# Kernel tuning notes

Hardware: AMD Instinct MI355X
Metric: run time of the kernel (lower is better)

The kernel has to match this reference:

```python
import jax, jax.numpy as jnp
import numpy as np
import math

B, SQ, SK = 8, 1024, 1024
DIM_Q = DIM_K = DIM_V = 512
H = 8
EPS = 1e-5
INF = jnp.float32(1e38)


def _ln(x, g, b):
    mu = jnp.mean(x, axis=-1, keepdims=True)
    var = jnp.mean(jnp.square(x - mu), axis=-1, keepdims=True)
    return (x - mu) * jax.lax.rsqrt(var + EPS) * g + b


def setup_inputs() -> dict:
    key = jax.random.key(0)
    ks = jax.random.split(key, 12)
    s = 1.0 / math.sqrt(DIM_V)
    return {
        "queries": jax.random.normal(ks[0], (B, SQ, DIM_Q), jnp.float32),
        "keys": jax.random.normal(ks[1], (B, SK, DIM_K), jnp.float32),
        # binary presence masks (as in the original usage)
        "presence_q": (jax.random.uniform(ks[2], (B, SQ)) > 0.1).astype(jnp.float32),
        "presence_k": (jax.random.uniform(ks[3], (B, SK)) > 0.1).astype(jnp.float32),
        "num_heads": H,
        "Wq": jax.random.normal(ks[4], (DIM_Q, DIM_V), jnp.float32) * s,
        "bq": jnp.zeros((DIM_V,), jnp.float32),
        "Wk": jax.random.normal(ks[5], (DIM_K, DIM_V), jnp.float32) * s,
        "bk": jnp.zeros((DIM_V,), jnp.float32),
        "Wv": jax.random.normal(ks[6], (DIM_K, DIM_V), jnp.float32) * s,
        "bv": jnp.zeros((DIM_V,), jnp.float32),
        "Wo": jax.random.normal(ks[7], (DIM_V, DIM_V), jnp.float32) * s,
        "bo": jnp.zeros((DIM_V,), jnp.float32),
        "g0": jnp.ones((DIM_V,), jnp.float32),
        "b0": jnp.zeros((DIM_V,), jnp.float32),
        "g1": jnp.ones((DIM_V,), jnp.float32),
        "b1": jnp.zeros((DIM_V,), jnp.float32),
    }


def reference(queries, keys, presence_q, presence_k, num_heads,
              Wq, bq, Wk, bk, Wv, bv, Wo, bo, g0, b0, g1, b1):
    b, sq, _ = queries.shape
    dim_v = Wq.shape[1]
    d = dim_v // num_heads
    q = queries @ Wq + bq                              # [B,Sq,V]
    k = keys @ Wk + bk                                 # [B,Sk,V]
    v = keys @ Wv + bv                                 # [B,Sk,V]
    qh = q.reshape(b, sq, num_heads, d)
    kh = k.reshape(b, -1, num_heads, d)
    vh = v.reshape(b, -1, num_heads, d)
    logits = jnp.einsum('bqhd,bkhd->bhqk', qh, kh) / jnp.float32(math.sqrt(dim_v))
    pq = presence_q[:, None, :, None]                  # [B,1,Sq,1]
    logits = pq * logits - (1.0 - pq) * INF
    pk = presence_k[:, None, None, :]                  # [B,1,1,Sk]
    logits = pk * logits - (1.0 - pk) * INF
    A = jax.nn.softmax(logits, axis=-1)                # [B,H,Sq,Sk]
    o = qh + jnp.einsum('bhqk,bkhd->bqhd', A, vh)      # residual add of Q_
    o = o.reshape(b, sq, dim_v)
    o = _ln(o, g0, b0)
    o = o + jax.nn.relu(o @ Wo + bo)
    o = _ln(o, g1, b1)
    return o
```

## Files before the change

### kernel.cpp

```cpp
#include <hip/hip_runtime.h>

typedef __attribute__((ext_vector_type(8))) short short8;
typedef __attribute__((ext_vector_type(4))) float f32x4;

#define SCALE2 0.06375871571f
#define C1     674.4237f

__device__ __forceinline__ float bfu(unsigned short u){
  return __uint_as_float(((unsigned int)u) << 16);
}
__device__ __forceinline__ unsigned short f2b(float x){
  unsigned int b = __float_as_uint(x);
  return (unsigned short)((b + 0x7fffu + ((b>>16)&1u)) >> 16);
}
__device__ __forceinline__ uint4 pack8(const float* f){
  float4 a = *(const float4*)f, b = *(const float4*)(f+4);
  uint4 r;
  r.x = (unsigned)f2b(a.x) | ((unsigned)f2b(a.y)<<16);
  r.y = (unsigned)f2b(a.z) | ((unsigned)f2b(a.w)<<16);
  r.z = (unsigned)f2b(b.x) | ((unsigned)f2b(b.y)<<16);
  r.w = (unsigned)f2b(b.z) | ((unsigned)f2b(b.w)<<16);
  return r;
}

__global__ __launch_bounds__(256) void prep_w(
    const float* Wq, const float* Wk, const float* Wv, const float* Wo,
    unsigned short* wt)
{
  const int m = blockIdx.z;
  const float* W = (m==0)?Wq:(m==1)?Wk:(m==2)?Wv:Wo;
  unsigned short* dst = wt + (long)m*262144;
  __shared__ unsigned short tile[64][72];
  const int t = threadIdx.x;
  const int n0 = blockIdx.x*64, k0 = blockIdx.y*64;
  {
    int r = t>>2, c0 = (t&3)*16;
    uint4 u0 = pack8(W + (long)(k0+r)*512 + n0 + c0);
    uint4 u1 = pack8(W + (long)(k0+r)*512 + n0 + c0 + 8);
    unsigned short* us0 = (unsigned short*)&u0;
    unsigned short* us1 = (unsigned short*)&u1;
    #pragma unroll
    for (int i=0;i<8;++i) tile[c0+i][r] = us0[i];
    #pragma unroll
    for (int i=0;i<8;++i) tile[c0+8+i][r] = us1[i];
  }
  __syncthreads();
  {
    int n = t>>2, ks = (t&3)*16;
    *(uint4*)(dst + (long)(n0+n)*512 + k0 + ks)     = *(uint4*)&tile[n][ks];
    *(uint4*)(dst + (long)(n0+n)*512 + k0 + ks + 8) = *(uint4*)&tile[n][ks+8];
  }
}

__global__ __launch_bounds__(256) void proj_mfma(
    const float* queries, const float* keys, const unsigned short* wt,
    const float* bq, const float* bk, const float* bv,
    unsigned short* q_bf, unsigned short* k_bf, unsigned short* vt_bf)
{
  const int mat = blockIdx.z;
  const float* A = (mat==0)? queries : keys;
  const unsigned short* Wt = wt + (long)mat*262144;
  const float* bias = (mat==0)?bq:(mat==1)?bk:bv;
  const int row0 = blockIdx.y*128, col0 = blockIdx.x*128;
  __shared__ unsigned short As[128][40];
  __shared__ unsigned short Ws[128][40];
  const int t = threadIdx.x;
  const int lane = t & 63, wid = t >> 6;
  const int ln = lane & 15, quad = lane >> 4;
  const int wy = wid >> 1, wx = wid & 1;
  f32x4 acc[4][4];
  #pragma unroll
  for (int i=0;i<4;++i){
    #pragma unroll
    for (int j=0;j<4;++j) acc[i][j] = (f32x4){0.f,0.f,0.f,0.f};
  }
  const int sr = t>>1, sk0 = (t&1)*16;
  for (int k0=0;k0<512;k0+=32){
    __syncthreads();
    {
      *(uint4*)&As[sr][sk0]   = pack8(A + (long)(row0+sr)*512 + k0 + sk0);
      *(uint4*)&As[sr][sk0+8] = pack8(A + (long)(row0+sr)*512 + k0 + sk0 + 8);
      *(uint4*)&Ws[sr][sk0]   = *(const uint4*)(Wt + (long)(col0+sr)*512 + k0 + sk0);
      *(uint4*)&Ws[sr][sk0+8] = *(const uint4*)(Wt + (long)(col0+sr)*512 + k0 + sk0 + 8);
    }
    __syncthreads();
    short8 a[4], b[4];
    #pragma unroll
    for (int mt=0;mt<4;++mt) a[mt] = *(const short8*)&As[wy*64+mt*16+ln][quad*8];
    #pragma unroll
    for (int nt=0;nt<4;++nt) b[nt] = *(const short8*)&Ws[wx*64+nt*16+ln][quad*8];
    #pragma unroll
    for (int mt=0;mt<4;++mt){
      #pragma unroll
      for (int nt=0;nt<4;++nt)
        acc[mt][nt] = __builtin_amdgcn_mfma_f32_16x16x32_bf16(a[mt], b[nt], acc[mt][nt], 0,0,0);
    }
  }
  float bias_v[4];
  #pragma unroll
  for (int nt=0;nt<4;++nt) bias_v[nt] = bias[col0 + wx*64 + nt*16 + ln];
  if (mat < 2){
    unsigned short* dst = (mat==0)? q_bf : k_bf;
    #pragma unroll
    for (int mt=0;mt<4;++mt){
      int row = row0 + wy*64 + mt*16 + quad*4;
      #pragma unroll
      for (int nt=0;nt<4;++nt){
        int col = col0 + wx*64 + nt*16 + ln;
        #pragma unroll
        for (int r=0;r<4;++r)
          dst[(long)(row+r)*512 + col] = f2b(acc[mt][nt][r] + bias_v[nt]);
      }
    }
  } else {
    #pragma unroll
    for (int mt=0;mt<4;++mt){
      int row = row0 + wy*64 + mt*16 + quad*4;
      int bb = row >> 10, sk = row & 1023;
      #pragma unroll
      for (int nt=0;nt<4;++nt){
        int col = col0 + wx*64 + nt*16 + ln;
        int h = col >> 6, dd = col & 63;
        uint2 pk2; unsigned short* pp = (unsigned short*)&pk2;
        #pragma unroll
        for (int r=0;r<4;++r) pp[r] = f2b(acc[mt][nt][r] + bias_v[nt]);
        *(uint2*)(vt_bf + (((long)((bb*8+h)*64+dd)) << 10) + sk) = pk2;
      }
    }
  }
}

__global__ __launch_bounds__(512) void attn_mfma(
    const unsigned short* q_bf, const unsigned short* k_bf, const unsigned short* vt_bf,
    const float* pres_q, const float* pres_k, float* o1)
{
  const int bx = blockIdx.x;
  const int b = bx >> 3, h = bx & 7;
  const int q0 = blockIdx.y * 128;
  const int t = threadIdx.x;
  const int lane = t & 63, wid = t >> 6, ln = lane & 15, quad = lane >> 4;
  __shared__ unsigned short Qs[128][72];
  __shared__ unsigned short Ks[64][72];
  __shared__ unsigned short Vt[64][72];
  __shared__ unsigned short Ps[128][72];
  __shared__ float pq_s[128], pk_s[64];
  {
    int tok = t>>2, ds = (t&3)*16;
    const unsigned short* src = q_bf + (long)(b*1024 + q0 + tok)*512 + h*64 + ds;
    *(uint4*)&Qs[tok][ds]   = *(const uint4*)src;
    *(uint4*)&Qs[tok][ds+8] = *(const uint4*)(src+8);
  }
  if (t < 128) pq_s[t] = pres_q[b*1024 + q0 + t];
  __syncthreads();
  short8 aq0 = *(const short8*)&Qs[wid*16+ln][quad*8];
  short8 aq1 = *(const short8*)&Qs[wid*16+ln][32+quad*8];
  float av[4];
  #pragma unroll
  for (int r=0;r<4;++r) av[r] = pq_s[wid*16 + quad*4 + r]*SCALE2;
  f32x4 oacc[4];
  #pragma unroll
  for (int dt=0;dt<4;++dt) oacc[dt] = (f32x4){0.f,0.f,0.f,0.f};
  float lsum[4] = {0.f,0.f,0.f,0.f};

  for (int k0=0;k0<1024;k0+=64){
    __syncthreads();
    {
      int tok = t>>3, ds = (t&7)*8;
      *(uint4*)&Ks[tok][ds] = *(const uint4*)(k_bf + (long)(b*1024 + k0 + tok)*512 + h*64 + ds);
      *(uint4*)&Vt[tok][ds] = *(const uint4*)(vt_bf + (((long)((b*8+h)*64 + tok)) << 10) + k0 + ds);
    }
    if (t < 64) pk_s[t] = pres_k[b*1024 + k0 + t];
    __syncthreads();
    f32x4 s[4];
    #pragma unroll
    for (int kt=0;kt<4;++kt) s[kt] = (f32x4){0.f,0.f,0.f,0.f};
    #pragma unroll
    for (int kt=0;kt<4;++kt){
      short8 kb0 = *(const short8*)&Ks[kt*16+ln][quad*8];
      short8 kb1 = *(const short8*)&Ks[kt*16+ln][32+quad*8];
      s[kt] = __builtin_amdgcn_mfma_f32_16x16x32_bf16(aq0, kb0, s[kt], 0,0,0);
      s[kt] = __builtin_amdgcn_mfma_f32_16x16x32_bf16(aq1, kb1, s[kt], 0,0,0);
    }
    float pk4[4];
    #pragma unroll
    for (int kt=0;kt<4;++kt) pk4[kt] = pk_s[kt*16+ln];
    #pragma unroll
    for (int r=0;r<4;++r){
      float sv[4];
      #pragma unroll
      for (int kt=0;kt<4;++kt){
        float a = av[r]*pk4[kt];
        float c = __builtin_fmaf(a, C1, -43.f);
        float x = __builtin_fmaf(s[kt][r], a, c);
        x = fminf(fmaxf(x, -100.f), 60.f);
        float e = __builtin_amdgcn_exp2f(x);
        lsum[r] += e;
        sv[kt] = e;
      }
      int prow = wid*16 + quad*4 + r;
      #pragma unroll
      for (int kt=0;kt<4;++kt) Ps[prow][kt*16+ln] = f2b(sv[kt]);
    }
    short8 ap0 = *(const short8*)&Ps[wid*16+ln][quad*8];
    short8 ap1 = *(const short8*)&Ps[wid*16+ln][32+quad*8];
    #pragma unroll
    for (int dt=0;dt<4;++dt){
      short8 vb0 = *(const short8*)&Vt[dt*16+ln][quad*8];
      short8 vb1 = *(const short8*)&Vt[dt*16+ln][32+quad*8];
      oacc[dt] = __builtin_amdgcn_mfma_f32_16x16x32_bf16(ap0, vb0, oacc[dt], 0,0,0);
      oacc[dt] = __builtin_amdgcn_mfma_f32_16x16x32_bf16(ap1, vb1, oacc[dt], 0,0,0);
    }
  }
  #pragma unroll
  for (int r=0;r<4;++r){
    float l = lsum[r];
    #pragma unroll
    for (int msk=1; msk<16; msk<<=1) l += __shfl_xor(l, msk);
    float inv = 1.f / l;
    int ql = wid*16 + quad*4 + r;
    long base = (long)(b*1024 + q0 + ql)*512 + h*64;
    #pragma unroll
    for (int dt=0;dt<4;++dt)
      o1[base + dt*16 + ln] = bfu(Qs[ql][dt*16+ln]) + oacc[dt][r]*inv;
  }
}

__global__ __launch_bounds__(256) void ln_kernel(
    const float* in, void* outp, int mode, const float* g, const float* bvec)
{
  const int row = blockIdx.x*4 + (threadIdx.x >> 6);
  const int lane = threadIdx.x & 63;
  const float* x = in + (long)row*512 + lane*8;
  float v[8];
  *(float4*)&v[0] = *(const float4*)x;
  *(float4*)&v[4] = *(const float4*)(x + 4);
  float sum = 0.f;
  #pragma unroll
  for (int c=0;c<8;++c) sum += v[c];
  #pragma unroll
  for (int msk=1; msk<64; msk<<=1) sum += __shfl_xor(sum, msk);
  float mu = sum * (1.f/512.f);
  float var = 0.f;
  #pragma unroll
  for (int c=0;c<8;++c){ v[c] -= mu; var += v[c]*v[c]; }
  #pragma unroll
  for (int msk=1; msk<64; msk<<=1) var += __shfl_xor(var, msk);
  float rs = rsqrtf(var*(1.f/512.f) + 1e-5f);
  float gv[8], bv[8];
  *(float4*)&gv[0] = *(const float4*)(g + lane*8);
  *(float4*)&gv[4] = *(const float4*)(g + lane*8 + 4);
  *(float4*)&bv[0] = *(const float4*)(bvec + lane*8);
  *(float4*)&bv[4] = *(const float4*)(bvec + lane*8 + 4);
  float y[8];
  #pragma unroll
  for (int c=0;c<8;++c) y[c] = v[c]*rs*gv[c] + bv[c];
  if (mode){
    float* dst = (float*)outp + (long)row*512 + lane*8;
    *(float4*)dst       = *(float4*)&y[0];
    *(float4*)(dst + 4) = *(float4*)&y[4];
  } else {
    uint4 out; unsigned short* os = (unsigned short*)&out;
    #pragma unroll
    for (int c=0;c<8;++c) os[c] = f2b(y[c]);
    *(uint4*)((unsigned short*)outp + (long)row*512 + lane*8) = out;
  }
}

__global__ __launch_bounds__(256) void out_mfma(
    const unsigned short* t_bf, const unsigned short* Wt, const float* bo,
    float* o1)
{
  const int row0 = blockIdx.y*128, col0 = blockIdx.x*128;
  __shared__ unsigned short As[128][40];
  __shared__ unsigned short Ws[128][40];
  const int t = threadIdx.x;
  const int lane = t & 63, wid = t >> 6;
  const int ln = lane & 15, quad = lane >> 4;
  const int wy = wid >> 1, wx = wid & 1;
  f32x4 acc[4][4];
  #pragma unroll
  for (int i=0;i<4;++i){
    #pragma unroll
    for (int j=0;j<4;++j) acc[i][j] = (f32x4){0.f,0.f,0.f,0.f};
  }
  const int sr = t>>1, sk0 = (t&1)*16;
  for (int k0=0;k0<512;k0+=32){
    __syncthreads();
    *(uint4*)&As[sr][sk0]   = *(const uint4*)(t_bf + (long)(row0+sr)*512 + k0 + sk0);
    *(uint4*)&As[sr][sk0+8] = *(const uint4*)(t_bf + (long)(row0+sr)*512 + k0 + sk0 + 8);
    *(uint4*)&Ws[sr][sk0]   = *(const uint4*)(Wt + (long)(col0+sr)*512 + k0 + sk0);
    *(uint4*)&Ws[sr][sk0+8] = *(const uint4*)(Wt + (long)(col0+sr)*512 + k0 + sk0 + 8);
    __syncthreads();
    short8 a[4], b[4];
    #pragma unroll
    for (int mt=0;mt<4;++mt) a[mt] = *(const short8*)&As[wy*64+mt*16+ln][quad*8];
    #pragma unroll
    for (int nt=0;nt<4;++nt) b[nt] = *(const short8*)&Ws[wx*64+nt*16+ln][quad*8];
    #pragma unroll
    for (int mt=0;mt<4;++mt){
      #pragma unroll
      for (int nt=0;nt<4;++nt)
        acc[mt][nt] = __builtin_amdgcn_mfma_f32_16x16x32_bf16(a[mt], b[nt], acc[mt][nt], 0,0,0);
    }
  }
  float bias_v[4];
  #pragma unroll
  for (int nt=0;nt<4;++nt) bias_v[nt] = bo[col0 + wx*64 + nt*16 + ln];
  #pragma unroll
  for (int mt=0;mt<4;++mt){
    int row = row0 + wy*64 + mt*16 + quad*4;
    #pragma unroll
    for (int nt=0;nt<4;++nt){
      int col = col0 + wx*64 + nt*16 + ln;
      #pragma unroll
      for (int r=0;r<4;++r){
        long idx = (long)(row+r)*512 + col;
        float u = acc[mt][nt][r] + bias_v[nt];
        u = fmaxf(u, 0.f);
        o1[idx] = bfu(t_bf[idx]) + u;
      }
    }
  }
}

extern "C" void kernel_launch(void* const* d_in, const int* in_sizes, int n_in,
                              void* d_out, int out_size, void* d_ws, size_t ws_size,
                              hipStream_t stream)
{
  unsigned short* q_bf  = (unsigned short*)d_ws;
  unsigned short* k_bf  = q_bf  + 8192l*512;
  unsigned short* vt_bf = k_bf  + 8192l*512;
  unsigned short* t_bf  = vt_bf + 8192l*512;
  unsigned short* wt    = t_bf  + 8192l*512;
  float* o1 = (float*)(wt + 4l*512*512);

  hipLaunchKernelGGL(prep_w, dim3(8,8,4), dim3(256), 0, stream,
                     (const float*)d_in[5], (const float*)d_in[7],
                     (const float*)d_in[9], (const float*)d_in[11], wt);
  hipLaunchKernelGGL(proj_mfma, dim3(4,64,3), dim3(256), 0, stream,
                     (const float*)d_in[0], (const float*)d_in[1], wt,
                     (const float*)d_in[6], (const float*)d_in[8],
                     (const float*)d_in[10], q_bf, k_bf, vt_bf);
  hipLaunchKernelGGL(attn_mfma, dim3(64,8), dim3(512), 0, stream,
                     q_bf, k_bf, vt_bf,
                     (const float*)d_in[2], (const float*)d_in[3], o1);
  hipLaunchKernelGGL(ln_kernel, dim3(2048), dim3(256), 0, stream,
                     o1, (void*)t_bf, 0, (const float*)d_in[13], (const float*)d_in[14]);
  hipLaunchKernelGGL(out_mfma, dim3(4,64), dim3(256), 0, stream,
                     t_bf, wt + 3l*512*512, (const float*)d_in[12], o1);
  hipLaunchKernelGGL(ln_kernel, dim3(2048), dim3(256), 0, stream,
                     o1, d_out, 1, (const float*)d_in[15], (const float*)d_in[16]);
}
```

Baseline: 221.5 us.

## Pre-convert inputs to bf16, double-buffer GEMM tiles, shrink out_mfma row tile

Adds a conv_bf kernel that converts queries and keys to bf16 once, into the o1 workspace, so proj_mfma no longer repacks fp32 for each of the three projections. proj_mfma and out_mfma now double-buffer their shared-memory tiles with register prefetch, overlapping global loads with MFMA and using one barrier per k-step. out_mfma uses 64-row tiles to launch twice as many blocks for better occupancy. The cost is an extra launch and extra memory traffic for the bf16 copies.

Measured after the change: 213.4 us. 1.04x faster.

```diff
diff --git a/kernel.cpp b/kernel.cpp
--- a/kernel.cpp
+++ b/kernel.cpp
@@ -21,6 +21,14 @@
   r.z = (unsigned)f2b(b.x) | ((unsigned)f2b(b.y)<<16);
   r.w = (unsigned)f2b(b.z) | ((unsigned)f2b(b.w)<<16);
   return r;
+}
+
+__global__ __launch_bounds__(256) void conv_bf(
+    const float* q, const float* k, unsigned short* dst)
+{
+  long i = ((long)blockIdx.x*256 + threadIdx.x)*8;
+  const float* src = (i < 4194304) ? q + i : k + (i - 4194304);
+  *(uint4*)(dst + i) = pack8(src);
 }
 
 __global__ __launch_bounds__(256) void prep_w(
@@ -53,17 +61,17 @@
 }
 
 __global__ __launch_bounds__(256) void proj_mfma(
-    const float* queries, const float* keys, const unsigned short* wt,
+    const unsigned short* qin, const unsigned short* kin, const unsigned short* wt,
     const float* bq, const float* bk, const float* bv,
     unsigned short* q_bf, unsigned short* k_bf, unsigned short* vt_bf)
 {
   const int mat = blockIdx.z;
-  const float* A = (mat==0)? queries : keys;
+  const unsigned short* A = (mat==0)? qin : kin;
   const unsigned short* Wt = wt + (long)mat*262144;
   const float* bias = (mat==0)?bq:(mat==1)?bk:bv;
   const int row0 = blockIdx.y*128, col0 = blockIdx.x*128;
-  __shared__ unsigned short As[128][40];
-  __shared__ unsigned short Ws[128][40];
+  __shared__ unsigned short As[2][128][40];
+  __shared__ unsigned short Ws[2][128][40];
   const int t = threadIdx.x;
   const int lane = t & 63, wid = t >> 6;
   const int ln = lane & 15, quad = lane >> 4;
@@ -75,26 +83,43 @@
     for (int j=0;j<4;++j) acc[i][j] = (f32x4){0.f,0.f,0.f,0.f};
   }
   const int sr = t>>1, sk0 = (t&1)*16;
-  for (int k0=0;k0<512;k0+=32){
-    __syncthreads();
-    {
-      *(uint4*)&As[sr][sk0]   = pack8(A + (long)(row0+sr)*512 + k0 + sk0);
-      *(uint4*)&As[sr][sk0+8] = pack8(A + (long)(row0+sr)*512 + k0 + sk0 + 8);
-      *(uint4*)&Ws[sr][sk0]   = *(const uint4*)(Wt + (long)(col0+sr)*512 + k0 + sk0);
-      *(uint4*)&Ws[sr][sk0+8] = *(const uint4*)(Wt + (long)(col0+sr)*512 + k0 + sk0 + 8);
-    }
-    __syncthreads();
+  const unsigned short* Arow = A  + (long)(row0+sr)*512 + sk0;
+  const unsigned short* Wrow = Wt + (long)(col0+sr)*512 + sk0;
+  uint4 a0 = *(const uint4*)(Arow);
+  uint4 a1 = *(const uint4*)(Arow + 8);
+  uint4 w0 = *(const uint4*)(Wrow);
+  uint4 w1 = *(const uint4*)(Wrow + 8);
+  *(uint4*)&As[0][sr][sk0]   = a0;
+  *(uint4*)&As[0][sr][sk0+8] = a1;
+  *(uint4*)&Ws[0][sr][sk0]   = w0;
+  *(uint4*)&Ws[0][sr][sk0+8] = w1;
+  __syncthreads();
+  for (int it=0; it<16; ++it){
+    const int cur = it & 1;
+    if (it < 15){
+      a0 = *(const uint4*)(Arow + (it+1)*32);
+      a1 = *(const uint4*)(Arow + (it+1)*32 + 8);
+      w0 = *(const uint4*)(Wrow + (it+1)*32);
+      w1 = *(const uint4*)(Wrow + (it+1)*32 + 8);
+    }
     short8 a[4], b[4];
     #pragma unroll
-    for (int mt=0;mt<4;++mt) a[mt] = *(const short8*)&As[wy*64+mt*16+ln][quad*8];
-    #pragma unroll
-    for (int nt=0;nt<4;++nt) b[nt] = *(const short8*)&Ws[wx*64+nt*16+ln][quad*8];
+    for (int mt=0;mt<4;++mt) a[mt] = *(const short8*)&As[cur][wy*64+mt*16+ln][quad*8];
+    #pragma unroll
+    for (int nt=0;nt<4;++nt) b[nt] = *(const short8*)&Ws[cur][wx*64+nt*16+ln][quad*8];
     #pragma unroll
     for (int mt=0;mt<4;++mt){
       #pragma unroll
       for (int nt=0;nt<4;++nt)
         acc[mt][nt] = __builtin_amdgcn_mfma_f32_16x16x32_bf16(a[mt], b[nt], acc[mt][nt], 0,0,0);
     }
+    if (it < 15){
+      *(uint4*)&As[cur^1][sr][sk0]   = a0;
+      *(uint4*)&As[cur^1][sr][sk0+8] = a1;
+      *(uint4*)&Ws[cur^1][sr][sk0]   = w0;
+      *(uint4*)&Ws[cur^1][sr][sk0+8] = w1;
+    }
+    __syncthreads();
   }
   float bias_v[4];
   #pragma unroll
@@ -270,45 +295,61 @@
     const unsigned short* t_bf, const unsigned short* Wt, const float* bo,
     float* o1)
 {
-  const int row0 = blockIdx.y*128, col0 = blockIdx.x*128;
-  __shared__ unsigned short As[128][40];
-  __shared__ unsigned short Ws[128][40];
+  const int row0 = blockIdx.y*64, col0 = blockIdx.x*128;
+  __shared__ unsigned short As[2][64][40];
+  __shared__ unsigned short Ws[2][128][40];
   const int t = threadIdx.x;
   const int lane = t & 63, wid = t >> 6;
   const int ln = lane & 15, quad = lane >> 4;
   const int wy = wid >> 1, wx = wid & 1;
-  f32x4 acc[4][4];
-  #pragma unroll
-  for (int i=0;i<4;++i){
+  f32x4 acc[2][4];
+  #pragma unroll
+  for (int i=0;i<2;++i){
     #pragma unroll
     for (int j=0;j<4;++j) acc[i][j] = (f32x4){0.f,0.f,0.f,0.f};
   }
-  const int sr = t>>1, sk0 = (t&1)*16;
-  for (int k0=0;k0<512;k0+=32){
-    __syncthreads();
-    *(uint4*)&As[sr][sk0]   = *(const uint4*)(t_bf + (long)(row0+sr)*512 + k0 + sk0);
-    *(uint4*)&As[sr][sk0+8] = *(const uint4*)(t_bf + (long)(row0+sr)*512 + k0 + sk0 + 8);
-    *(uint4*)&Ws[sr][sk0]   = *(const uint4*)(Wt + (long)(col0+sr)*512 + k0 + sk0);
-    *(uint4*)&Ws[sr][sk0+8] = *(const uint4*)(Wt + (long)(col0+sr)*512 + k0 + sk0 + 8);
-    __syncthreads();
-    short8 a[4], b[4];
-    #pragma unroll
-    for (int mt=0;mt<4;++mt) a[mt] = *(const short8*)&As[wy*64+mt*16+ln][quad*8];
-    #pragma unroll
-    for (int nt=0;nt<4;++nt) b[nt] = *(const short8*)&Ws[wx*64+nt*16+ln][quad*8];
-    #pragma unroll
-    for (int mt=0;mt<4;++mt){
+  const int ar = t>>2, ac0 = (t&3)*8;
+  const int wr = t>>1, wc0 = (t&1)*16;
+  const unsigned short* Arow = t_bf + (long)(row0+ar)*512 + ac0;
+  const unsigned short* Wrow = Wt   + (long)(col0+wr)*512 + wc0;
+  uint4 a0 = *(const uint4*)(Arow);
+  uint4 w0 = *(const uint4*)(Wrow);
+  uint4 w1 = *(const uint4*)(Wrow + 8);
+  *(uint4*)&As[0][ar][ac0] = a0;
+  *(uint4*)&Ws[0][wr][wc0]   = w0;
+  *(uint4*)&Ws[0][wr][wc0+8] = w1;
+  __syncthreads();
+  for (int it=0; it<16; ++it){
+    const int cur = it & 1;
+    if (it < 15){
+      a0 = *(const uint4*)(Arow + (it+1)*32);
+      w0 = *(const uint4*)(Wrow + (it+1)*32);
+      w1 = *(const uint4*)(Wrow + (it+1)*32 + 8);
+    }
+    short8 a[2], b[4];
+    #pragma unroll
+    for (int mt=0;mt<2;++mt) a[mt] = *(const short8*)&As[cur][wy*32+mt*16+ln][quad*8];
+    #pragma unroll
+    for (int nt=0;nt<4;++nt) b[nt] = *(const short8*)&Ws[cur][wx*64+nt*16+ln][quad*8];
+    #pragma unroll
+    for (int mt=0;mt<2;++mt){
       #pragma unroll
       for (int nt=0;nt<4;++nt)
         acc[mt][nt] = __builtin_amdgcn_mfma_f32_16x16x32_bf16(a[mt], b[nt], acc[mt][nt], 0,0,0);
     }
+    if (it < 15){
+      *(uint4*)&As[cur^1][ar][ac0] = a0;
+      *(uint4*)&Ws[cur^1][wr][wc0]   = w0;
+      *(uint4*)&Ws[cur^1][wr][wc0+8] = w1;
+    }
+    __syncthreads();
   }
   float bias_v[4];
   #pragma unroll
   for (int nt=0;nt<4;++nt) bias_v[nt] = bo[col0 + wx*64 + nt*16 + ln];
   #pragma unroll
-  for (int mt=0;mt<4;++mt){
-    int row = row0 + wy*64 + mt*16 + quad*4;
+  for (int mt=0;mt<2;++mt){
+    int row = row0 + wy*32 + mt*16 + quad*4;
     #pragma unroll
     for (int nt=0;nt<4;++nt){
       int col = col0 + wx*64 + nt*16 + ln;
@@ -333,12 +374,16 @@
   unsigned short* t_bf  = vt_bf + 8192l*512;
   unsigned short* wt    = t_bf  + 8192l*512;
   float* o1 = (float*)(wt + 4l*512*512);
-
+  unsigned short* qin = (unsigned short*)o1;
+  unsigned short* kin = qin + 4194304;
+
+  hipLaunchKernelGGL(conv_bf, dim3(4096), dim3(256), 0, stream,
+                     (const float*)d_in[0], (const float*)d_in[1], qin);
   hipLaunchKernelGGL(prep_w, dim3(8,8,4), dim3(256), 0, stream,
                      (const float*)d_in[5], (const float*)d_in[7],
                      (const float*)d_in[9], (const float*)d_in[11], wt);
   hipLaunchKernelGGL(proj_mfma, dim3(4,64,3), dim3(256), 0, stream,
-                     (const float*)d_in[0], (const float*)d_in[1], wt,
+                     qin, kin, wt,
                      (const float*)d_in[6], (const float*)d_in[8],
                      (const float*)d_in[10], q_bf, k_bf, vt_bf);
   hipLaunchKernelGGL(attn_mfma, dim3(64,8), dim3(512), 0, stream,
@@ -346,7 +391,7 @@
                      (const float*)d_in[2], (const float*)d_in[3], o1);
   hipLaunchKernelGGL(ln_kernel, dim3(2048), dim3(256), 0, stream,
                      o1, (void*)t_bf, 0, (const float*)d_in[13], (const float*)d_in[14]);
-  hipLaunchKernelGGL(out_mfma, dim3(4,64), dim3(256), 0, stream,
+  hipLaunchKernelGGL(out_mfma, dim3(4,128), dim3(256), 0, stream,
                      t_bf, wt + 3l*512*512, (const float*)d_in[12], o1);
   hipLaunchKernelGGL(ln_kernel, dim3(2048), dim3(256), 0, stream,
                      o1, d_out, 1, (const float*)d_in[15], (const float*)d_in[16]);
```
